# Kernel tuning notes

Measured on AMD Instinct MI355X. Metric: run time of the kernel, lower is better.

Reference implementation:

```python
import jax, jax.numpy as jnp
import numpy as np

B, N, M, D = 2, 16384, 4096, 128  # batch, points, voxels, d_model (= d_points)


def _mlp(x, W1, b1, W2, b2):
    # Linear -> ReLU -> Linear (matches nn.Sequential(Linear, ReLU, Linear))
    return jax.nn.relu(x @ W1 + b1) @ W2 + b2


def setup_inputs() -> dict:
    key = jax.random.key(0)
    ks = jax.random.split(key, 12)
    s = 0.02
    inp = {
        "p_xyz": jax.random.normal(ks[0], (B, N, 3), jnp.float32),
        "v_xyz": jax.random.normal(ks[1], (B, 3), jnp.float32),
        "p_features": jax.random.normal(ks[2], (B, N, D), jnp.float32),
        "v_featrues": jax.random.normal(ks[3], (B, M, D), jnp.float32),
    }

    def two_layer(k, din):
        k1, k2 = jax.random.split(k)
        return (jax.random.normal(k1, (din, D), jnp.float32) * s,
                jnp.zeros((D,), jnp.float32),
                jax.random.normal(k2, (D, D), jnp.float32) * s,
                jnp.zeros((D,), jnp.float32))

    for name, din, k in (("alpha", D, ks[4]), ("beta", D, ks[5]),
                         ("omega", D, ks[6]), ("delta", 3, ks[7])):
        W1, b1, W2, b2 = two_layer(k, din)
        inp[name + "_W1"] = W1
        inp[name + "_b1"] = b1
        inp[name + "_W2"] = W2
        inp[name + "_b2"] = b2
    return inp


def reference(p_xyz, v_xyz, p_features, v_featrues,
              alpha_W1, alpha_b1, alpha_W2, alpha_b2,
              beta_W1, beta_b1, beta_W2, beta_b2,
              omega_W1, omega_b1, omega_W2, omega_b2,
              delta_W1, delta_b1, delta_W2, delta_b2):
    # dist = |p_xyz - v_xyz| per batch: [B, N, 3]
    dist = jnp.abs(p_xyz - v_xyz[:, None, :])
    pv = _mlp(dist, delta_W1, delta_b1, delta_W2, delta_b2)        # [B, N, D]
    q = _mlp(v_featrues, alpha_W1, alpha_b1, alpha_W2, alpha_b2)   # [B, M, D]
    k = _mlp(p_features, beta_W1, beta_b1, beta_W2, beta_b2)       # [B, N, D]
    v = _mlp(p_features, omega_W1, omega_b1, omega_W2, omega_b2)   # [B, N, D]
    # q@k^T + q@pv^T == q@(k+pv)^T : [B, M, N]
    scale = 1.0 / jnp.sqrt(jnp.asarray(D, dtype=q.dtype))
    scores = jnp.einsum('bmd,bnd->bmn', q, k + pv) * scale
    # softmax over dim=-2 (the query/voxel dim M), as in the original
    w = jax.nn.softmax(scores, axis=-2)                            # [B, M, N]
    res = jnp.einsum('bmn,bnd->bmd', w, v)                         # [B, M, D]
    return res + v_featrues
```

## Files before the change

kernel.cpp:

```cpp
#include <hip/hip_runtime.h>

#define B_ 2
#define N_ 16384
#define M_ 4096
#define D_ 128

typedef __attribute__((ext_vector_type(8))) short s8;
typedef __attribute__((ext_vector_type(4))) float f4;
typedef __attribute__((ext_vector_type(16))) float f16v;
typedef __attribute__((ext_vector_type(4))) unsigned short us4;
typedef unsigned short u16;

__device__ __forceinline__ u16 f2b(float f) {
  unsigned int x = __float_as_uint(f);
  unsigned int r = x + 0x7fffu + ((x >> 16) & 1u);
  return (u16)(r >> 16);
}
__device__ __forceinline__ s8 ld8(const u16* p) {
  return *reinterpret_cast<const s8*>(p);
}
__device__ __forceinline__ s8 ldcvt8(const float* p) {
  f4 x = *reinterpret_cast<const f4*>(p);
  f4 y = *reinterpret_cast<const f4*>(p + 4);
  s8 r;
  r[0] = (short)f2b(x[0]); r[1] = (short)f2b(x[1]);
  r[2] = (short)f2b(x[2]); r[3] = (short)f2b(x[3]);
  r[4] = (short)f2b(y[0]); r[5] = (short)f2b(y[1]);
  r[6] = (short)f2b(y[2]); r[7] = (short)f2b(y[3]);
  return r;
}
__device__ __forceinline__ f4 mfma16(s8 a, s8 b, f4 c) {
  return __builtin_amdgcn_mfma_f32_16x16x32_bf16(a, b, c, 0, 0, 0);
}
__device__ __forceinline__ f16v mfma32(s8 a, s8 b, f16v c) {
  return __builtin_amdgcn_mfma_f32_32x32x16_bf16(a, b, c, 0, 0, 0);
}
__device__ __forceinline__ int swz(int row, int off) {
  return (row << 8) + ((((off >> 4) ^ (row & 15)) << 4) | (off & 15));
}
#define CS 0.1275174365f

__global__ __launch_bounds__(256) void wtrans(
    const float* a0, const float* a1, const float* a2, const float* a3,
    const float* a4, const float* a5, const float* a6, u16* dst) {
  const int mat = blockIdx.x >> 4, part = blockIdx.x & 15;
  const float* s;
  switch (mat) {
    case 0: s = a0; break; case 1: s = a1; break; case 2: s = a2; break;
    case 3: s = a3; break; case 4: s = a4; break; case 5: s = a5; break;
    default: s = a6; break;
  }
  u16* d = dst + mat * 16384 + part * 1024;
  const int o0 = part * 1024;
  for (int i = threadIdx.x; i < 1024; i += 256) {
    const int o = o0 + i;
    const int c = o >> 7, r = o & 127;
    d[i] = f2b(s[r * 128 + c]);
  }
}

__global__ __launch_bounds__(256) void mlps(
    const float* __restrict__ vfeat,
    const u16* __restrict__ aW1t, const float* __restrict__ ab1,
    const u16* __restrict__ aW2t, const float* __restrict__ ab2,
    u16* __restrict__ qbuf,
    const float* __restrict__ pf, const float* __restrict__ pxyz,
    const float* __restrict__ vxyz,
    const u16* __restrict__ bW1t, const float* __restrict__ bb1,
    const u16* __restrict__ bW2t, const float* __restrict__ bb2,
    const float* __restrict__ dW1, const float* __restrict__ db1,
    const u16* __restrict__ dW2t, const float* __restrict__ db2,
    const u16* __restrict__ oW1t, const float* __restrict__ ob1,
    const u16* __restrict__ oW2t, const float* __restrict__ ob2,
    u16* __restrict__ kpv_out, u16* __restrict__ vt_out) {
  __shared__ u16 H1[64][136];
  __shared__ u16 H2[64][136];
  __shared__ u16 H3[64][136];
  const int tid = threadIdx.x;
  const int wave = tid >> 6, lane = tid & 63;
  const int c16 = lane & 15, quad = lane >> 4;

  if (blockIdx.x < 256) {
    const int rowg = wave & 1, nsh = wave >> 1;
    const long row0 = (long)blockIdx.x * 32 + rowg * 16;
    s8 a[4];
    {
      const float* xr = vfeat + (row0 + c16) * D_ + quad * 8;
      #pragma unroll
      for (int kk = 0; kk < 4; kk++) a[kk] = ldcvt8(xr + kk * 32);
    }
    #pragma unroll
    for (int ns = 0; ns < 4; ns++) {
      f4 acc = {0.f, 0.f, 0.f, 0.f};
      const int c = (nsh * 4 + ns) * 16 + c16;
      const u16* wr = aW1t + (long)c * 128 + quad * 8;
      #pragma unroll
      for (int kk = 0; kk < 4; kk++) acc = mfma16(a[kk], ld8(wr + kk * 32), acc);
      const float bias = ab1[c];
      #pragma unroll
      for (int r = 0; r < 4; r++) {
        float v = acc[r] + bias;
        H1[rowg * 16 + quad * 4 + r][c] = f2b(v > 0.f ? v : 0.f);
      }
    }
    __syncthreads();
    s8 a2[4];
    #pragma unroll
    for (int kk = 0; kk < 4; kk++)
      a2[kk] = *reinterpret_cast<const s8*>(&H1[rowg * 16 + c16][kk * 32 + quad * 8]);
    #pragma unroll
    for (int ns = 0; ns < 4; ns++) {
      f4 acc = {0.f, 0.f, 0.f, 0.f};
      const int c = (nsh * 4 + ns) * 16 + c16;
      const u16* wr = aW2t + (long)c * 128 + quad * 8;
      #pragma unroll
      for (int kk = 0; kk < 4; kk++) acc = mfma16(a2[kk], ld8(wr + kk * 32), acc);
      const float bias = ab2[c];
      #pragma unroll
      for (int r = 0; r < 4; r++)
        qbuf[(row0 + quad * 4 + r) * D_ + c] = f2b(acc[r] + bias);
    }
    return;
  }
  const int bx = blockIdx.x - 256;
  const long row0 = (long)bx * 64 + wave * 16;
  s8 a[4];
  {
    const float* xr = pf + (row0 + c16) * D_ + quad * 8;
    #pragma unroll
    for (int kk = 0; kk < 4; kk++) a[kk] = ldcvt8(xr + kk * 32);
  }
  #pragma unroll
  for (int ns = 0; ns < 8; ns++) {
    f4 accb = {0.f, 0.f, 0.f, 0.f}, acco = {0.f, 0.f, 0.f, 0.f};
    const int c = ns * 16 + c16;
    const u16* wrb = bW1t + (long)c * 128 + quad * 8;
    const u16* wro = oW1t + (long)c * 128 + quad * 8;
    #pragma unroll
    for (int kk = 0; kk < 4; kk++) {
      accb = mfma16(a[kk], ld8(wrb + kk * 32), accb);
      acco = mfma16(a[kk], ld8(wro + kk * 32), acco);
    }
    const float biasb = bb1[c], biaso = ob1[c];
    #pragma unroll
    for (int r = 0; r < 4; r++) {
      float vb = accb[r] + biasb;
      float vo = acco[r] + biaso;
      H1[wave * 16 + quad * 4 + r][c] = f2b(vb > 0.f ? vb : 0.f);
      H3[wave * 16 + quad * 4 + r][c] = f2b(vo > 0.f ? vo : 0.f);
    }
  }
  {
    const long bat = ((long)bx * 64) / N_;
    const float vx0 = vxyz[bat * 3 + 0];
    const float vx1 = vxyz[bat * 3 + 1];
    const float vx2 = vxyz[bat * 3 + 2];
    for (int i = 0; i < 32; i++) {
      const int e = lane + 64 * i;
      const int rr = e >> 7, cc = e & 127;
      const long gr = row0 + rr;
      const float d0 = fabsf(pxyz[gr * 3 + 0] - vx0);
      const float d1 = fabsf(pxyz[gr * 3 + 1] - vx1);
      const float d2 = fabsf(pxyz[gr * 3 + 2] - vx2);
      float h = d0 * dW1[cc] + d1 * dW1[128 + cc] + d2 * dW1[256 + cc] + db1[cc];
      H2[wave * 16 + rr][cc] = f2b(h > 0.f ? h : 0.f);
    }
  }
  __syncthreads();
  s8 ab[4], ad[4], ao[4];
  #pragma unroll
  for (int kk = 0; kk < 4; kk++) {
    ab[kk] = *reinterpret_cast<const s8*>(&H1[wave * 16 + c16][kk * 32 + quad * 8]);
    ad[kk] = *reinterpret_cast<const s8*>(&H2[wave * 16 + c16][kk * 32 + quad * 8]);
    ao[kk] = *reinterpret_cast<const s8*>(&H3[wave * 16 + c16][kk * 32 + quad * 8]);
  }
  #pragma unroll
  for (int ns = 0; ns < 8; ns++) {
    const int c = ns * 16 + c16;
    f4 acck = {0.f, 0.f, 0.f, 0.f};
    f4 accv = {0.f, 0.f, 0.f, 0.f};
    const u16* wrb = bW2t + (long)c * 128 + quad * 8;
    const u16* wrd = dW2t + (long)c * 128 + quad * 8;
    const u16* wro = oW2t + (long)c * 128 + quad * 8;
    #pragma unroll
    for (int kk = 0; kk < 4; kk++) {
      acck = mfma16(ab[kk], ld8(wrb + kk * 32), acck);
      acck = mfma16(ad[kk], ld8(wrd + kk * 32), acck);
      accv = mfma16(ao[kk], ld8(wro + kk * 32), accv);
    }
    const float biask = bb2[c] + db2[c];
    const float biasv = ob2[c];
    #pragma unroll
    for (int r = 0; r < 4; r++)
      kpv_out[(row0 + quad * 4 + r) * D_ + c] = f2b(acck[r] + biask);
    {
      const long g = row0 + quad * 4;
      const long bb = g >> 14;
      const long n = g & (N_ - 1);
      us4 pk;
      #pragma unroll
      for (int r = 0; r < 4; r++) pk[r] = f2b(accv[r] + biasv);
      *reinterpret_cast<us4*>(vt_out + bb * (long)128 * N_ + (long)c * N_ + n) = pk;
    }
  }
}

__global__ __launch_bounds__(512, 6) void colsum_v2c(const u16* __restrict__ q,
    const u16* __restrict__ kpv, float* __restrict__ sums) {
  __shared__ char LQ[16384];
  const int tid = threadIdx.x;
  const int wave = tid >> 6, lane = tid & 63;
  const int c16 = lane & 15, quad = lane >> 4;
  const int mh = blockIdx.x & 3;
  const int nb = ((blockIdx.x >> 2) & 127) * 128 + wave * 16;
  const int b = blockIdx.x >> 9;
  const int rsub = lane >> 4, ch = lane & 15;

  s8 ak[4];
  {
    const u16* kr = kpv + ((long)b * N_ + nb + c16) * D_ + quad * 8;
    #pragma unroll
    for (int kk = 0; kk < 4; kk++) ak[kk] = ld8(kr + kk * 32);
  }
  f4 sum = {0.f, 0.f, 0.f, 0.f};
  const u16* qb = q + (long)b * M_ * D_ + (long)mh * (M_ / 4) * D_;

  for (int m0 = 0; m0 < M_ / 4; m0 += 64) {
    s8 t0 = ld8(qb + (long)(m0 + wave * 8 + rsub) * D_ + ch * 8);
    s8 t1 = ld8(qb + (long)(m0 + wave * 8 + 4 + rsub) * D_ + ch * 8);
    *reinterpret_cast<s8*>(LQ + swz(wave * 8 + rsub, ch * 16)) = t0;
    *reinterpret_cast<s8*>(LQ + swz(wave * 8 + 4 + rsub, ch * 16)) = t1;
    __syncthreads();
    #pragma unroll
    for (int ms = 0; ms < 4; ms++) {
      f4 st = {0.f, 0.f, 0.f, 0.f};
      #pragma unroll
      for (int kk = 0; kk < 4; kk++) {
        s8 bq = *reinterpret_cast<const s8*>(LQ + swz(ms * 16 + c16, kk * 64 + quad * 16));
        st = mfma16(ak[kk], bq, st);
      }
      #pragma unroll
      for (int r = 0; r < 4; r++) sum[r] += exp2f(st[r] * CS);
    }
    __syncthreads();
  }
  #pragma unroll
  for (int mask = 1; mask < 16; mask <<= 1) {
    #pragma unroll
    for (int r = 0; r < 4; r++) sum[r] += __shfl_xor(sum[r], mask, 64);
  }
  if (c16 == 0)
    *reinterpret_cast<f4*>(sums + (long)mh * (B_ * N_) + (long)b * N_ + nb + quad * 4) = sum;
}

__global__ __launch_bounds__(256) void recip_k(const float* __restrict__ sums,
                                               float* __restrict__ l2ic) {
  const int i = blockIdx.x * 256 + threadIdx.x;
  const float s = sums[i] + sums[B_ * N_ + i] + sums[2 * B_ * N_ + i]
                + sums[3 * B_ * N_ + i];
  l2ic[i] = -log2f(s);
}

__global__ __launch_bounds__(256, 4) void attn_v7(const u16* __restrict__ q,
    const u16* __restrict__ kpv, const u16* __restrict__ vt,
    const float* __restrict__ l2ic, float* __restrict__ part,
    int lgns, int nslice) {
  __shared__ char LK[16384];
  __shared__ char LP[8192];
  const int tid = threadIdx.x;
  const int wave = tid >> 6, lane = tid & 63;
  const int l31 = lane & 31, hi = lane >> 5;
  const int bid = blockIdx.x;
  const int ns = bid & ((1 << lgns) - 1);
  const int mb = (bid >> lgns) & 63;
  const int b = bid >> (lgns + 6);
  const int nt = wave & 1, mt = wave >> 1;
  const int m_base = mb * 64;
  const int n_begin = ns * nslice;
  const int rsub = lane >> 4, ch = lane & 15;

  const u16* kpb = kpv + (long)b * N_ * D_;
  const u16* vtb = vt + (long)b * (long)D_ * N_;
  const float* l2b = l2ic + (long)b * N_;

  s8 bq[8];
  {
    const u16* qr = q + ((long)b * M_ + m_base + mt * 32 + l31) * D_ + hi * 8;
    #pragma unroll
    for (int kk = 0; kk < 8; kk++) bq[kk] = ld8(qr + kk * 16);
  }
  f16v acc[2];
  #pragma unroll
  for (int i = 0; i < 2; i++)
    #pragma unroll
    for (int r = 0; r < 16; r++) acc[i][r] = 0.f;

  s8 tmp[4];
  #pragma unroll
  for (int i = 0; i < 4; i++)
    tmp[i] = ld8(kpb + (long)(n_begin + wave * 16 + i * 4 + rsub) * D_ + ch * 8);

  for (int n0 = n_begin; n0 < n_begin + nslice; n0 += 64) {
    #pragma unroll
    for (int i = 0; i < 4; i++)
      *reinterpret_cast<s8*>(LK + swz(wave * 16 + i * 4 + rsub, ch * 16)) = tmp[i];
    {
      int nn = n0 + 64;
      if (nn >= n_begin + nslice) nn = n_begin;
      #pragma unroll
      for (int i = 0; i < 4; i++)
        tmp[i] = ld8(kpb + (long)(nn + wave * 16 + i * 4 + rsub) * D_ + ch * 8);
    }
    __syncthreads();
    {
      f16v st;
      #pragma unroll
      for (int r = 0; r < 16; r++) st[r] = 0.f;
      #pragma unroll
      for (int kk = 0; kk < 8; kk++) {
        s8 aK = *reinterpret_cast<const s8*>(
            LK + swz(nt * 32 + l31, kk * 32 + hi * 16));
        st = mfma32(aK, bq[kk], st);
      }
      #pragma unroll
      for (int g = 0; g < 4; g++) {
        const f4 l2 = *reinterpret_cast<const f4*>(l2b + n0 + nt * 32 + 8 * g + 4 * hi);
        us4 pk;
        #pragma unroll
        for (int r = 0; r < 4; r++)
          pk[r] = (u16)(__float_as_uint(exp2f(fmaf(st[g * 4 + r], CS, l2[r]))) >> 16);
        *reinterpret_cast<us4*>(LP + (4 * nt + g) * 1024 + (mt * 32 + l31) * 16 + 8 * hi) = pk;
      }
    }
    __syncthreads();
    #pragma unroll
    for (int kk = 0; kk < 4; kk++) {
      s8 bv = ld8(vtb + (long)(wave * 32 + l31) * N_ + n0 + kk * 16 + hi * 8);
      #pragma unroll
      for (int i = 0; i < 2; i++) {
        s8 ap = *reinterpret_cast<const s8*>(
            LP + (2 * kk + hi) * 1024 + (i * 32 + l31) * 16);
        acc[i] = mfma32(ap, bv, acc[i]);
      }
    }
  }
  float* pt = part + (long)bid * 64 * 128;
  #pragma unroll
  for (int i = 0; i < 2; i++)
    #pragma unroll
    for (int g = 0; g < 4; g++)
      #pragma unroll
      for (int r = 0; r < 4; r++)
        pt[(i * 32 + g * 8 + 4 * hi + r) * 128 + wave * 32 + l31] = acc[i][g * 4 + r];
}

__global__ __launch_bounds__(256) void attn_reduce(const float* __restrict__ part,
    const float* __restrict__ vfeat, float* __restrict__ out, int nsplit) {
  const int g4 = blockIdx.x * 256 + threadIdx.x;
  const int b = g4 >> 17;
  const int rem = g4 & 131071;
  const int m = rem >> 5;
  const int d4 = rem & 31;
  const int mb = m >> 6, mr = m & 63;
  const long base = ((long)(b * 64 + mb) * nsplit) * 8192 + mr * 128 + d4 * 4;
  f4 s = *reinterpret_cast<const f4*>(vfeat + (long)g4 * 4);
  for (int ns = 0; ns < nsplit; ns++)
    s += *reinterpret_cast<const f4*>(part + base + ns * 8192);
  *reinterpret_cast<f4*>(out + (long)g4 * 4) = s;
}

extern "C" void kernel_launch(void* const* d_in, const int* in_sizes, int n_in,
                              void* d_out, int out_size, void* d_ws, size_t ws_size,
                              hipStream_t stream) {
  const float* p_xyz  = (const float*)d_in[0];
  const float* v_xyz  = (const float*)d_in[1];
  const float* p_feat = (const float*)d_in[2];
  const float* v_feat = (const float*)d_in[3];
  const float* aW1 = (const float*)d_in[4],  *ab1 = (const float*)d_in[5];
  const float* aW2 = (const float*)d_in[6],  *ab2 = (const float*)d_in[7];
  const float* bW1 = (const float*)d_in[8],  *bb1 = (const float*)d_in[9];
  const float* bW2 = (const float*)d_in[10], *bb2 = (const float*)d_in[11];
  const float* oW1 = (const float*)d_in[12], *ob1 = (const float*)d_in[13];
  const float* oW2 = (const float*)d_in[14], *ob2 = (const float*)d_in[15];
  const float* dW1 = (const float*)d_in[16], *db1 = (const float*)d_in[17];
  const float* dW2 = (const float*)d_in[18], *db2 = (const float*)d_in[19];

  char* ws = (char*)d_ws;
  u16* wt    = (u16*)ws;
  u16* aW1t  = wt + 0 * 16384;
  u16* aW2t  = wt + 1 * 16384;
  u16* bW1t  = wt + 2 * 16384;
  u16* bW2t  = wt + 3 * 16384;
  u16* oW1t  = wt + 4 * 16384;
  u16* oW2t  = wt + 5 * 16384;
  u16* dW2t  = wt + 6 * 16384;
  u16* qbuf  = (u16*)(ws + 262144);
  u16* kpvb  = (u16*)(ws + 2359296);
  u16* vtb   = (u16*)(ws + 10747904);
  float* invb = (float*)(ws + 19136512);
  float* partb = (float*)(ws + 19267584);
  float* sums  = partb;

  const size_t part_off = 19267584;
  int lgns = (ws_size >= part_off + (size_t)8 * B_ * M_ * D_ * 4) ? 3 : 2;
  const int nsplit = 1 << lgns;
  const int nslice = N_ / nsplit;

  wtrans<<<dim3(112), dim3(256), 0, stream>>>(aW1, aW2, bW1, bW2, oW1, oW2, dW2, wt);
  mlps<<<dim3(256 + (B_ * N_) / 64), dim3(256), 0, stream>>>(
      v_feat, aW1t, ab1, aW2t, ab2, qbuf,
      p_feat, p_xyz, v_xyz, bW1t, bb1, bW2t, bb2, dW1, db1, dW2t, db2,
      oW1t, ob1, oW2t, ob2, kpvb, vtb);
  colsum_v2c<<<dim3(B_ * 128 * 4), dim3(512), 0, stream>>>(qbuf, kpvb, sums);
  recip_k<<<dim3((B_ * N_) / 256), dim3(256), 0, stream>>>(sums, invb);
  attn_v7<<<dim3(B_ * 64 * nsplit), dim3(256), 0, stream>>>(qbuf, kpvb, vtb, invb, partb,
                                                            lgns, nslice);
  attn_reduce<<<dim3((B_ * M_ * D_ / 4) / 256), dim3(256), 0, stream>>>(partb, v_feat,
                                                                        (float*)d_out,
                                                                        nsplit);
}
```

Baseline: 325.2 us.

## Load K fragments directly from global and double-buffer P tile with one barrier

The attention kernel stops staging K+pv tiles through shared memory and has each wave read its MFMA A-fragments straight from global memory. The P tile in LDS is double-buffered so only one barrier per iteration is needed instead of two. V loads are hoisted ahead of the barrier, and setprio brackets the MFMA sections. This removes LDS traffic and one sync per step, but K is now read redundantly by waves that share rows, and global load latency is exposed before the first MFMA.

```diff
diff --git a/kernel.cpp b/kernel.cpp
--- a/kernel.cpp
+++ b/kernel.cpp
@@ -261,12 +261,11 @@
   l2ic[i] = -log2f(s);
 }
 
-__global__ __launch_bounds__(256, 4) void attn_v7(const u16* __restrict__ q,
+__global__ __launch_bounds__(256, 4) void attn_v8(const u16* __restrict__ q,
     const u16* __restrict__ kpv, const u16* __restrict__ vt,
     const float* __restrict__ l2ic, float* __restrict__ part,
     int lgns, int nslice) {
-  __shared__ char LK[16384];
-  __shared__ char LP[8192];
+  __shared__ char LP[2][8192];
   const int tid = threadIdx.x;
   const int wave = tid >> 6, lane = tid & 63;
   const int l31 = lane & 31, hi = lane >> 5;
@@ -277,7 +276,6 @@
   const int nt = wave & 1, mt = wave >> 1;
   const int m_base = mb * 64;
   const int n_begin = ns * nslice;
-  const int rsub = lane >> 4, ch = lane & 15;
 
   const u16* kpb = kpv + (long)b * N_ * D_;
   const u16* vtb = vt + (long)b * (long)D_ * N_;
@@ -295,54 +293,49 @@
     #pragma unroll
     for (int r = 0; r < 16; r++) acc[i][r] = 0.f;
 
-  s8 tmp[4];
-  #pragma unroll
-  for (int i = 0; i < 4; i++)
-    tmp[i] = ld8(kpb + (long)(n_begin + wave * 16 + i * 4 + rsub) * D_ + ch * 8);
-
+  int lpo = 0;
   for (int n0 = n_begin; n0 < n_begin + nslice; n0 += 64) {
-    #pragma unroll
-    for (int i = 0; i < 4; i++)
-      *reinterpret_cast<s8*>(LK + swz(wave * 16 + i * 4 + rsub, ch * 16)) = tmp[i];
+    f16v st;
+    #pragma unroll
+    for (int r = 0; r < 16; r++) st[r] = 0.f;
     {
-      int nn = n0 + 64;
-      if (nn >= n_begin + nslice) nn = n_begin;
-      #pragma unroll
-      for (int i = 0; i < 4; i++)
-        tmp[i] = ld8(kpb + (long)(nn + wave * 16 + i * 4 + rsub) * D_ + ch * 8);
-    }
-    __syncthreads();
-    {
-      f16v st;
-      #pragma unroll
-      for (int r = 0; r < 16; r++) st[r] = 0.f;
-      #pragma unroll
-      for (int kk = 0; kk < 8; kk++) {
-        s8 aK = *reinterpret_cast<const s8*>(
-            LK + swz(nt * 32 + l31, kk * 32 + hi * 16));
-        st = mfma32(aK, bq[kk], st);
-      }
-      #pragma unroll
-      for (int g = 0; g < 4; g++) {
-        const f4 l2 = *reinterpret_cast<const f4*>(l2b + n0 + nt * 32 + 8 * g + 4 * hi);
-        us4 pk;
-        #pragma unroll
-        for (int r = 0; r < 4; r++)
-          pk[r] = (u16)(__float_as_uint(exp2f(fmaf(st[g * 4 + r], CS, l2[r]))) >> 16);
-        *reinterpret_cast<us4*>(LP + (4 * nt + g) * 1024 + (mt * 32 + l31) * 16 + 8 * hi) = pk;
-      }
-    }
-    __syncthreads();
+      const u16* kr = kpb + (long)(n0 + nt * 32 + l31) * D_ + hi * 8;
+      __builtin_amdgcn_s_setprio(1);
+      #pragma unroll
+      for (int kk = 0; kk < 8; kk++) st = mfma32(ld8(kr + kk * 16), bq[kk], st);
+      __builtin_amdgcn_s_setprio(0);
+    }
+    #pragma unroll
+    for (int g = 0; g < 4; g++) {
+      const f4 l2 = *reinterpret_cast<const f4*>(l2b + n0 + nt * 32 + 8 * g + 4 * hi);
+      us4 pk;
+      #pragma unroll
+      for (int r = 0; r < 4; r++)
+        pk[r] = (u16)(__float_as_uint(exp2f(fmaf(st[g * 4 + r], CS, l2[r]))) >> 16);
+      *reinterpret_cast<us4*>(LP[0] + lpo + (4 * nt + g) * 1024
+                              + (mt * 32 + l31) * 16 + 8 * hi) = pk;
+    }
+    s8 bv[4];
+    #pragma unroll
+    for (int kk = 0; kk < 4; kk++)
+      bv[kk] = ld8(vtb + (long)(wave * 32 + l31) * N_ + n0 + kk * 16 + hi * 8);
+    __builtin_amdgcn_sched_barrier(0);
+    asm volatile("s_waitcnt lgkmcnt(0)");
+    __builtin_amdgcn_sched_barrier(0);
+    __builtin_amdgcn_s_barrier();
+    __builtin_amdgcn_sched_barrier(0);
+    __builtin_amdgcn_s_setprio(1);
     #pragma unroll
     for (int kk = 0; kk < 4; kk++) {
-      s8 bv = ld8(vtb + (long)(wave * 32 + l31) * N_ + n0 + kk * 16 + hi * 8);
       #pragma unroll
       for (int i = 0; i < 2; i++) {
         s8 ap = *reinterpret_cast<const s8*>(
-            LP + (2 * kk + hi) * 1024 + (i * 32 + l31) * 16);
-        acc[i] = mfma32(ap, bv, acc[i]);
+            LP[0] + lpo + (2 * kk + hi) * 1024 + (i * 32 + l31) * 16);
+        acc[i] = mfma32(ap, bv[kk], acc[i]);
       }
     }
+    __builtin_amdgcn_s_setprio(0);
+    lpo ^= 8192;
   }
   float* pt = part + (long)bid * 64 * 128;
   #pragma unroll
@@ -413,7 +406,7 @@
       oW1t, ob1, oW2t, ob2, kpvb, vtb);
   colsum_v2c<<<dim3(B_ * 128 * 4), dim3(512), 0, stream>>>(qbuf, kpvb, sums);
   recip_k<<<dim3((B_ * N_) / 256), dim3(256), 0, stream>>>(sums, invb);
-  attn_v7<<<dim3(B_ * 64 * nsplit), dim3(256), 0, stream>>>(qbuf, kpvb, vtb, invb, partb,
+  attn_v8<<<dim3(B_ * 64 * nsplit), dim3(256), 0, stream>>>(qbuf, kpvb, vtb, invb, partb,
                                                             lgns, nslice);
   attn_reduce<<<dim3((B_ * M_ * D_ / 4) / 256), dim3(256), 0, stream>>>(partb, v_feat,
                                                                         (float*)d_out,
```

New measurement: 398.8 us. +22.6%, slower.
